# Kernel optimization log

Hardware: AMD Instinct MI355X
Metric: run time of the kernel (lower is better)

## Reference

```python
import jax, jax.numpy as jnp
import numpy as np

HEAD = 4

def setup_inputs() -> dict:
    key = jax.random.key(0)
    ks = jax.random.split(key, 6)
    b, h, w, dim, attn_dim = 2, 64, 64, 256, 128
    return {
        "query": jax.random.normal(ks[0], (b, h, w, dim), jnp.float32),
        "context": jax.random.normal(ks[1], (b, h, w, dim), jnp.float32),
        "Wq": jax.random.normal(ks[2], (dim, attn_dim), jnp.float32) * (dim ** -0.5),
        "Wk": jax.random.normal(ks[3], (dim, attn_dim), jnp.float32) * (dim ** -0.5),
        "Wv": jax.random.normal(ks[4], (dim, attn_dim), jnp.float32) * (dim ** -0.5),
        "Wo": jax.random.normal(ks[5], (attn_dim, dim), jnp.float32) * (attn_dim ** -0.5),
    }

def reference(query, context, Wq, Wk, Wv, Wo):
    b, h, w, c = query.shape
    attn_dim = Wq.shape[1]
    head = HEAD
    head_dim = attn_dim // head
    scale = head_dim ** -0.5
    n = h * w
    # 1x1 conv, no bias == per-pixel dense projection
    q = (query.reshape(b, n, c) @ Wq).reshape(b, n, head, head_dim)
    k = (context.reshape(b, n, c) @ Wk).reshape(b, n, head, head_dim)
    v = (context.reshape(b, n, c) @ Wv).reshape(b, n, head, head_dim)
    score = jnp.einsum('bihd,bjhd->bijh', q, k) * scale  # [b, n, n, head]
    attn = jax.nn.softmax(score, axis=-2)  # softmax over key axis j
    out = jnp.einsum('bijh,bjhd->bihd', attn, v).reshape(b, n, attn_dim)
    return (out @ Wo).reshape(b, h, w, c)
```

## Files before the change

kernel.cpp:

```cpp
#include <hip/hip_runtime.h>
#include <hip/hip_bf16.h>
#include <math.h>

#define N_TOK 4096
#define C_DIM 256
#define A_DIM 128
#define HEADS 4
#define HD    32
#define NBAT  2
#define BH    (NBAT * HEADS)

#define SCALE_LOG2E 0.25503521f

#define SPLITS 8
#define KEYS_PER_SPLIT (N_TOK / SPLITS)

typedef __attribute__((ext_vector_type(8))) short short8;
typedef __attribute__((ext_vector_type(4))) short short4_t;
typedef __attribute__((ext_vector_type(4))) float floatx4;

__device__ __forceinline__ unsigned short f2bf(float f) {
    unsigned int u = __float_as_uint(f);
    u = (u + 0x7fffu + ((u >> 16) & 1u)) >> 16;
    return (unsigned short)u;
}
__device__ __forceinline__ float bf2f(unsigned short u) {
    return __uint_as_float((unsigned int)u << 16);
}
__device__ __forceinline__ unsigned int pack2(float a, float b) {
    unsigned int lo = (__float_as_uint(a) + 0x8000u) >> 16;
    unsigned int hi = (__float_as_uint(b) + 0x8000u) & 0xffff0000u;
    return hi | lo;
}

__device__ __forceinline__ short8 quad_xpose(unsigned int a0, unsigned int a1,
                                             unsigned int a2, unsigned int a3,
                                             int lane)
{
    union { unsigned int u[4]; short8 s; } cv;
#if __has_builtin(__builtin_amdgcn_permlane32_swap) && __has_builtin(__builtin_amdgcn_permlane16_swap)
    (void)lane;
    auto s0 = __builtin_amdgcn_permlane32_swap(a0, a2, false, false);
    auto s1 = __builtin_amdgcn_permlane32_swap(a1, a3, false, false);
    auto t0 = __builtin_amdgcn_permlane16_swap(s0[0], s0[1], false, false);
    auto t1 = __builtin_amdgcn_permlane16_swap(s1[0], s1[1], false, false);
    cv.u[0] = t0[0]; cv.u[1] = t1[0]; cv.u[2] = t0[1]; cv.u[3] = t1[1];
#else
    const int hi32 = (lane >> 5) & 1;
    const int u16  = (lane >> 4) & 1;
    unsigned int x0 = __shfl_xor(a2, 32), x2 = __shfl_xor(a0, 32);
    unsigned int r0 = hi32 ? x0 : a0;
    unsigned int r1 = hi32 ? a2 : x2;
    unsigned int y0 = __shfl_xor(a3, 32), y2 = __shfl_xor(a1, 32);
    unsigned int r0b = hi32 ? y0 : a1;
    unsigned int r1b = hi32 ? a3 : y2;
    unsigned int w0 = (unsigned int)__builtin_amdgcn_ds_swizzle((int)r1, 0x401F);
    unsigned int w1 = (unsigned int)__builtin_amdgcn_ds_swizzle((int)r0, 0x401F);
    unsigned int w2 = (unsigned int)__builtin_amdgcn_ds_swizzle((int)r1b, 0x401F);
    unsigned int w3 = (unsigned int)__builtin_amdgcn_ds_swizzle((int)r0b, 0x401F);
    cv.u[0] = u16 ? w0 : r0;
    cv.u[1] = u16 ? w2 : r0b;
    cv.u[2] = u16 ? r1 : w1;
    cv.u[3] = u16 ? r1b : w3;
#endif
    return cv.s;
}

__global__ __launch_bounds__(256) void wpack_kernel(
    const float* __restrict__ Wq, const float* __restrict__ Wk,
    const float* __restrict__ Wv, const float* __restrict__ Wo,
    unsigned short* __restrict__ Wp)
{
    const int chunk = blockIdx.x * 256 + threadIdx.x;
    const int wid = chunk >> 12;
    const int c = chunk & 4095;
    const int lane = c & 63, quad = lane >> 4, l15 = lane & 15;
    short8 v;
    if (wid < 3) {
        const int s = c >> 9, t = (c >> 6) & 7;
        const float* W = (wid == 0) ? Wq : ((wid == 1) ? Wk : Wv);
        const float scale = (wid == 0) ? SCALE_LOG2E : 1.0f;
        const int src = (s * 32 + quad * 8) * A_DIM + t * 16 + l15;
        #pragma unroll
        for (int j = 0; j < 8; j++) v[j] = (short)f2bf(W[src + j * A_DIM] * scale);
    } else {
        const int s = c >> 10, t = (c >> 6) & 15;
        const int src = (s * 32 + quad * 8) * C_DIM + t * 16 + l15;
        #pragma unroll
        for (int j = 0; j < 8; j++) v[j] = (short)f2bf(Wo[src + j * C_DIM]);
    }
    *(short8*)(Wp + (long)chunk * 8) = v;
}

__global__ __launch_bounds__(256) void qkv_kernel(
    const float* __restrict__ query, const float* __restrict__ context,
    const unsigned short* __restrict__ Wp,
    unsigned short* __restrict__ Qb, unsigned short* __restrict__ Kb,
    unsigned short* __restrict__ Vb)
{
    __shared__ __align__(16) unsigned short V_lds[128 * 18];

    const int tid = threadIdx.x;
    const int w = tid >> 6, lane = tid & 63;
    const int quad = lane >> 4, l15 = lane & 15;
    const int ch = w;
    const long i0 = (long)blockIdx.x * 16;
    const long row = i0 + l15;

    const unsigned short* Wqp = Wp;
    const unsigned short* Wkp = Wp + 32768;
    const unsigned short* Wvp = Wp + 65536;

    floatx4 aQ[2] = {}, aK[2] = {}, aV[2] = {};

    for (int s = 0; s < 8; s++) {
        const float* qp = query + row * C_DIM + s * 32 + quad * 8;
        const float* cp = context + row * C_DIM + s * 32 + quad * 8;
        floatx4 q0 = *(const floatx4*)qp, q1 = *(const floatx4*)(qp + 4);
        floatx4 c0 = *(const floatx4*)cp, c1 = *(const floatx4*)(cp + 4);
        short8 aq, ac;
        #pragma unroll
        for (int j = 0; j < 4; j++) {
            aq[j] = (short)f2bf(q0[j]); aq[4 + j] = (short)f2bf(q1[j]);
            ac[j] = (short)f2bf(c0[j]); ac[4 + j] = (short)f2bf(c1[j]);
        }
        #pragma unroll
        for (int tp = 0; tp < 2; tp++) {
            const long fo = ((long)(s * 8 + ch * 2 + tp) * 64 + lane) * 8;
            short8 bq = *(const short8*)(Wqp + fo);
            short8 bk = *(const short8*)(Wkp + fo);
            short8 bv = *(const short8*)(Wvp + fo);
            aQ[tp] = __builtin_amdgcn_mfma_f32_16x16x32_bf16(aq, bq, aQ[tp], 0, 0, 0);
            aK[tp] = __builtin_amdgcn_mfma_f32_16x16x32_bf16(ac, bk, aK[tp], 0, 0, 0);
            aV[tp] = __builtin_amdgcn_mfma_f32_16x16x32_bf16(ac, bv, aV[tp], 0, 0, 0);
        }
    }

    const long b = i0 >> 12;
    const long n0 = i0 & (N_TOK - 1);
    const long nbase = n0 + quad * 4;
    #pragma unroll
    for (int tp = 0; tp < 2; tp++) {
        const int col = ch * 32 + tp * 16 + l15;
        const int h = col >> 5, d = col & 31;
        unsigned short* qdst = Qb + ((b * HEADS + h) * N_TOK + nbase) * HD + d;
        unsigned short* kdst = Kb + ((b * HEADS + h) * N_TOK + nbase) * HD + d;
        #pragma unroll
        for (int r = 0; r < 4; r++) {
            qdst[r * HD] = f2bf(aQ[tp][r]);
            kdst[r * HD] = f2bf(aK[tp][r]);
        }
        short4_t pv;
        #pragma unroll
        for (int r = 0; r < 4; r++) pv[r] = (short)f2bf(aV[tp][r]);
        *(short4_t*)&V_lds[col * 18 + quad * 4] = pv;
    }
    __syncthreads();

    {
        const int col = tid >> 1, seg = tid & 1;
        const int h = col >> 5, d = col & 31;
        unsigned short* dst = Vb + ((b * HEADS + h) * HD + d) * N_TOK + n0 + seg * 8;
        *(short8*)dst = *(const short8*)&V_lds[col * 18 + seg * 8];
    }
}

__global__ __launch_bounds__(256, 4) void attn_kernel(
    const unsigned short* __restrict__ Qb, const unsigned short* __restrict__ Kb,
    const unsigned short* __restrict__ Vb,
    unsigned short* __restrict__ AO, float* __restrict__ Lbuf)
{
    const int tid  = threadIdx.x;
    const int w    = tid >> 6;
    const int lane = tid & 63;
    const int quad = lane >> 4;
    const int l15  = lane & 15;

    const int L  = blockIdx.x;
    const int g  = (L & 7) + 8 * ((L >> 3) >> 5);
    const int qb = (L >> 3) & 31;
    const int bh = g & 7;
    const int z  = g >> 3;
    const int i0 = qb * 128 + w * 32;

    const unsigned short* Qh = Qb + (long)bh * N_TOK * HD;
    const unsigned short* Kh = Kb + (long)bh * N_TOK * HD;
    const unsigned short* Vh = Vb + (long)bh * HD * N_TOK;

    const short8 qfA = *(const short8*)(Qh + (long)(i0 + l15) * HD + quad * 8);
    const short8 qfB = *(const short8*)(Qh + (long)(i0 + 16 + l15) * HD + quad * 8);

    floatx4 accA0 = {0.f,0.f,0.f,0.f}, accA1 = {0.f,0.f,0.f,0.f};
    floatx4 accB0 = {0.f,0.f,0.f,0.f}, accB1 = {0.f,0.f,0.f,0.f};
    float lAc = 0.f, lBc = 0.f;

    const int j_lo = z * KEYS_PER_SPLIT;

    const unsigned short* kp  = Kh + (long)j_lo * HD + l15 * HD + quad * 8;
    const unsigned short* vp0 = Vh + (long)l15 * N_TOK + j_lo + quad * 8;
    const unsigned short* vp1 = vp0 + 16 * N_TOK;

    #pragma unroll 1
    for (int t = 0; t < KEYS_PER_SPLIT / 64; ++t) {
        const short8 k00 = *(const short8*)(kp);
        const short8 k10 = *(const short8*)(kp + 16 * HD);
        const short8 k01 = *(const short8*)(kp + 32 * HD);
        const short8 k11 = *(const short8*)(kp + 48 * HD);
        const short8 v00 = *(const short8*)(vp0);
        const short8 v10 = *(const short8*)(vp1);
        const short8 v01 = *(const short8*)(vp0 + 32);
        const short8 v11 = *(const short8*)(vp1 + 32);
        kp += 64 * HD; vp0 += 64; vp1 += 64;

        #pragma unroll
        for (int sub = 0; sub < 2; sub++) {
            const short8 kf0 = sub ? k01 : k00;
            const short8 kf1 = sub ? k11 : k10;
            const short8 vf0 = sub ? v01 : v00;
            const short8 vf1 = sub ? v11 : v10;

            const floatx4 zf = {0.f,0.f,0.f,0.f};
            floatx4 sA0 = __builtin_amdgcn_mfma_f32_16x16x32_bf16(kf0, qfA, zf, 0, 0, 0);
            floatx4 sA1 = __builtin_amdgcn_mfma_f32_16x16x32_bf16(kf1, qfA, zf, 0, 0, 0);
            floatx4 sB0 = __builtin_amdgcn_mfma_f32_16x16x32_bf16(kf0, qfB, zf, 0, 0, 0);
            floatx4 sB1 = __builtin_amdgcn_mfma_f32_16x16x32_bf16(kf1, qfB, zf, 0, 0, 0);

            floatx4 pA0, pA1, pB0, pB1;
            #pragma unroll
            for (int r = 0; r < 4; r++) {
                pA0[r] = __builtin_amdgcn_exp2f(sA0[r]);
                pA1[r] = __builtin_amdgcn_exp2f(sA1[r]);
                pB0[r] = __builtin_amdgcn_exp2f(sB0[r]);
                pB1[r] = __builtin_amdgcn_exp2f(sB1[r]);
                lAc += pA0[r] + pA1[r];
                lBc += pB0[r] + pB1[r];
            }

            short8 pfA = quad_xpose(pack2(pA0[0], pA0[1]), pack2(pA0[2], pA0[3]),
                                    pack2(pA1[0], pA1[1]), pack2(pA1[2], pA1[3]), lane);
            short8 pfB = quad_xpose(pack2(pB0[0], pB0[1]), pack2(pB0[2], pB0[3]),
                                    pack2(pB1[0], pB1[1]), pack2(pB1[2], pB1[3]), lane);

            accA0 = __builtin_amdgcn_mfma_f32_16x16x32_bf16(pfA, vf0, accA0, 0, 0, 0);
            accA1 = __builtin_amdgcn_mfma_f32_16x16x32_bf16(pfA, vf1, accA1, 0, 0, 0);
            accB0 = __builtin_amdgcn_mfma_f32_16x16x32_bf16(pfB, vf0, accB0, 0, 0, 0);
            accB1 = __builtin_amdgcn_mfma_f32_16x16x32_bf16(pfB, vf1, accB1, 0, 0, 0);
        }
    }

    lAc += __shfl_xor(lAc, 16); lAc += __shfl_xor(lAc, 32);
    lBc += __shfl_xor(lBc, 16); lBc += __shfl_xor(lBc, 32);

    const int b = bh >> 2, h = bh & 3;
    unsigned short* AOz = AO + (long)z * (NBAT * N_TOK * A_DIM);
    float* Lz = Lbuf + (long)z * (BH * N_TOK);
    if (quad == 0) {
        Lz[(long)bh * N_TOK + i0 + l15]      = lAc;
        Lz[(long)bh * N_TOK + i0 + 16 + l15] = lBc;
    }
    #pragma unroll
    for (int r = 0; r < 4; r++) {
        const float invA = 1.0f / __shfl(lAc, quad * 4 + r);
        const float invB = 1.0f / __shfl(lBc, quad * 4 + r);
        const long rowA = (long)b * N_TOK + i0 + quad * 4 + r;
        const long rowB = rowA + 16;
        AOz[rowA * A_DIM + h * HD + l15]      = f2bf(accA0[r] * invA);
        AOz[rowA * A_DIM + h * HD + 16 + l15] = f2bf(accA1[r] * invA);
        AOz[rowB * A_DIM + h * HD + l15]      = f2bf(accB0[r] * invB);
        AOz[rowB * A_DIM + h * HD + 16 + l15] = f2bf(accB1[r] * invB);
    }
}

__global__ __launch_bounds__(256) void outproj_kernel(
    const unsigned short* __restrict__ AO, const float* __restrict__ Lbuf,
    const unsigned short* __restrict__ Wp, float* __restrict__ out)
{
    const int tid = threadIdx.x;
    const int w = tid >> 6, lane = tid & 63;
    const int quad = lane >> 4, l15 = lane & 15;
    const int ch = w;
    const long i0 = (long)blockIdx.x * 16;
    const long row = i0 + l15;
    const int b = (int)(row >> 12);
    const int n = (int)(row & (N_TOK - 1));
    const unsigned short* Wop = Wp + 98304;

    floatx4 acc[4] = {};

    #pragma unroll
    for (int s = 0; s < 4; s++) {
        float lz[SPLITS], lsum = 0.f;
        #pragma unroll
        for (int z = 0; z < SPLITS; z++) {
            lz[z] = Lbuf[(long)z * (BH * N_TOK) + (long)(b * HEADS + s) * N_TOK + n];
            lsum += lz[z];
        }
        const float inv = 1.0f / lsum;
        float vals[8] = {};
        #pragma unroll
        for (int z = 0; z < SPLITS; z++) {
            short8 az = *(const short8*)(AO + (long)z * (NBAT * N_TOK * A_DIM) +
                                         row * A_DIM + s * 32 + quad * 8);
            const float wz = lz[z] * inv;
            #pragma unroll
            for (int j = 0; j < 8; j++) vals[j] += wz * bf2f((unsigned short)az[j]);
        }
        short8 af;
        #pragma unroll
        for (int j = 0; j < 8; j++) af[j] = (short)f2bf(vals[j]);
        #pragma unroll
        for (int tp = 0; tp < 4; tp++) {
            const int t = ch * 4 + tp;
            short8 bo = *(const short8*)(Wop + ((long)(s * 16 + t) * 64 + lane) * 8);
            acc[tp] = __builtin_amdgcn_mfma_f32_16x16x32_bf16(af, bo, acc[tp], 0, 0, 0);
        }
    }

    #pragma unroll
    for (int tp = 0; tp < 4; tp++) {
        #pragma unroll
        for (int r = 0; r < 4; r++)
            out[(i0 + quad * 4 + r) * C_DIM + (ch * 4 + tp) * 16 + l15] = acc[tp][r];
    }
}

extern "C" void kernel_launch(void* const* d_in, const int* in_sizes, int n_in,
                              void* d_out, int out_size, void* d_ws, size_t ws_size,
                              hipStream_t stream)
{
    const float* query   = (const float*)d_in[0];
    const float* context = (const float*)d_in[1];
    const float* Wq      = (const float*)d_in[2];
    const float* Wk      = (const float*)d_in[3];
    const float* Wv      = (const float*)d_in[4];
    const float* Wo      = (const float*)d_in[5];
    float* out = (float*)d_out;

    char* ws = (char*)d_ws;
    unsigned short* Qb = (unsigned short*)(ws);
    unsigned short* Kb = (unsigned short*)(ws + (2 << 20));
    unsigned short* Vb = (unsigned short*)(ws + (4 << 20));
    unsigned short* AO = (unsigned short*)(ws + (6 << 20));
    float*          Lb = (float*)(ws + (22 << 20));
    unsigned short* Wp = (unsigned short*)(ws + (23 << 20));

    wpack_kernel<<<dim3(64), dim3(256), 0, stream>>>(Wq, Wk, Wv, Wo, Wp);
    qkv_kernel<<<dim3(512), dim3(256), 0, stream>>>(query, context, Wp, Qb, Kb, Vb);
    attn_kernel<<<dim3(32 * BH * SPLITS), dim3(256), 0, stream>>>(
        Qb, Kb, Vb, AO, Lb);
    outproj_kernel<<<dim3(512), dim3(256), 0, stream>>>(AO, Lb, Wp, out);
}
```

Before: 148.0 us.

## Stage K/V tiles through double-buffered LDS with register prefetch

```diff
diff --git a/kernel.cpp b/kernel.cpp
--- a/kernel.cpp
+++ b/kernel.cpp
@@ -14,6 +14,9 @@
 
 #define SPLITS 8
 #define KEYS_PER_SPLIT (N_TOK / SPLITS)
+
+#define KS 40
+#define VS 72
 
 typedef __attribute__((ext_vector_type(8))) short short8;
 typedef __attribute__((ext_vector_type(4))) short short4_t;
@@ -170,6 +173,9 @@
     const unsigned short* __restrict__ Vb,
     unsigned short* __restrict__ AO, float* __restrict__ Lbuf)
 {
+    __shared__ __align__(16) unsigned short K_lds[2][64 * KS];
+    __shared__ __align__(16) unsigned short V_lds[2][HD * VS];
+
     const int tid  = threadIdx.x;
     const int w    = tid >> 6;
     const int lane = tid & 63;
@@ -194,31 +200,30 @@
     floatx4 accB0 = {0.f,0.f,0.f,0.f}, accB1 = {0.f,0.f,0.f,0.f};
     float lAc = 0.f, lBc = 0.f;
 
+    const int  kst = (tid >> 2) * KS + (tid & 3) * 8;
+    const int  vst = (tid >> 3) * VS + (tid & 7) * 8;
+    const long vgl = (long)(tid >> 3) * N_TOK + (tid & 7) * 8;
+
     const int j_lo = z * KEYS_PER_SPLIT;
-
-    const unsigned short* kp  = Kh + (long)j_lo * HD + l15 * HD + quad * 8;
-    const unsigned short* vp0 = Vh + (long)l15 * N_TOK + j_lo + quad * 8;
-    const unsigned short* vp1 = vp0 + 16 * N_TOK;
+    const int nt   = KEYS_PER_SPLIT / 64;
+
+    short8 kreg = *(const short8*)(Kh + (long)j_lo * HD + tid * 8);
+    short8 vreg = *(const short8*)(Vh + vgl + j_lo);
+    *(short8*)&K_lds[0][kst] = kreg;
+    *(short8*)&V_lds[0][vst] = vreg;
+    kreg = *(const short8*)(Kh + (long)(j_lo + 64) * HD + tid * 8);
+    vreg = *(const short8*)(Vh + vgl + j_lo + 64);
+    __syncthreads();
 
     #pragma unroll 1
-    for (int t = 0; t < KEYS_PER_SPLIT / 64; ++t) {
-        const short8 k00 = *(const short8*)(kp);
-        const short8 k10 = *(const short8*)(kp + 16 * HD);
-        const short8 k01 = *(const short8*)(kp + 32 * HD);
-        const short8 k11 = *(const short8*)(kp + 48 * HD);
-        const short8 v00 = *(const short8*)(vp0);
-        const short8 v10 = *(const short8*)(vp1);
-        const short8 v01 = *(const short8*)(vp0 + 32);
-        const short8 v11 = *(const short8*)(vp1 + 32);
-        kp += 64 * HD; vp0 += 64; vp1 += 64;
+    for (int t = 0; t < nt; ++t) {
+        const int cur = t & 1;
 
         #pragma unroll
         for (int sub = 0; sub < 2; sub++) {
-            const short8 kf0 = sub ? k01 : k00;
-            const short8 kf1 = sub ? k11 : k10;
-            const short8 vf0 = sub ? v01 : v00;
-            const short8 vf1 = sub ? v11 : v10;
-
+            const int jb = sub * 32;
+            short8 kf0 = *(short8*)&K_lds[cur][(jb + l15) * KS + quad * 8];
+            short8 kf1 = *(short8*)&K_lds[cur][(jb + 16 + l15) * KS + quad * 8];
             const floatx4 zf = {0.f,0.f,0.f,0.f};
             floatx4 sA0 = __builtin_amdgcn_mfma_f32_16x16x32_bf16(kf0, qfA, zf, 0, 0, 0);
             floatx4 sA1 = __builtin_amdgcn_mfma_f32_16x16x32_bf16(kf1, qfA, zf, 0, 0, 0);
@@ -241,10 +246,22 @@
             short8 pfB = quad_xpose(pack2(pB0[0], pB0[1]), pack2(pB0[2], pB0[3]),
                                     pack2(pB1[0], pB1[1]), pack2(pB1[2], pB1[3]), lane);
 
+            short8 vf0 = *(short8*)&V_lds[cur][l15 * VS + jb + quad * 8];
+            short8 vf1 = *(short8*)&V_lds[cur][(16 + l15) * VS + jb + quad * 8];
             accA0 = __builtin_amdgcn_mfma_f32_16x16x32_bf16(pfA, vf0, accA0, 0, 0, 0);
             accA1 = __builtin_amdgcn_mfma_f32_16x16x32_bf16(pfA, vf1, accA1, 0, 0, 0);
             accB0 = __builtin_amdgcn_mfma_f32_16x16x32_bf16(pfB, vf0, accB0, 0, 0, 0);
             accB1 = __builtin_amdgcn_mfma_f32_16x16x32_bf16(pfB, vf1, accB1, 0, 0, 0);
+        }
+
+        if (t + 1 < nt) {
+            *(short8*)&K_lds[cur ^ 1][kst] = kreg;
+            *(short8*)&V_lds[cur ^ 1][vst] = vreg;
+            if (t + 2 < nt) {
+                kreg = *(const short8*)(Kh + (long)(j_lo + (t + 2) * 64) * HD + tid * 8);
+                vreg = *(const short8*)(Vh + vgl + j_lo + (t + 2) * 64);
+            }
+            __syncthreads();
         }
     }
 
```

New measurement: 130.0 us. 12.2% less time.
